# Performance work log

Hardware: AMD Instinct MI355X
Metric: run time of the kernel (lower is better)

## Reference

```python
import jax, jax.numpy as jnp
import numpy as np

N_INST = 100000
N_NET = 100000
E = 1600000
H = 64
OUT = 32
L = 2


def setup_inputs() -> dict:
    key = jax.random.key(0)
    ks = jax.random.split(key, 16)
    inp = {
        "x_inst": jax.random.normal(ks[0], (N_INST, H), jnp.float32),
        "x_net": jax.random.normal(ks[1], (N_NET, H), jnp.float32),
        "edge_i2n": jax.random.randint(ks[2], (2, E), 0, N_INST, jnp.int32),
        "edge_n2i": jax.random.randint(ks[3], (2, E), 0, N_NET, jnp.int32),
        # stacked GAT params: axis0 = layer, axis1 = relation (0: inst->net, 1: net->inst)
        "W_src": jax.random.normal(ks[4], (L, 2, H, H), jnp.float32) * 0.1,
        "W_dst": jax.random.normal(ks[5], (L, 2, H, H), jnp.float32) * 0.1,
        "att_src": jax.random.normal(ks[6], (L, 2, H), jnp.float32) * 0.1,
        "att_dst": jax.random.normal(ks[7], (L, 2, H), jnp.float32) * 0.1,
        "bias_g": jax.random.normal(ks[8], (L, 2, H), jnp.float32) * 0.1,
        "lin1_w": jax.random.normal(ks[9], (H, OUT), jnp.float32) * 0.1,
        "lin1_b": jax.random.normal(ks[10], (OUT,), jnp.float32) * 0.1,
        "lin2_w": jax.random.normal(ks[11], (OUT, 1), jnp.float32) * 0.1,
        "lin2_b": jax.random.normal(ks[12], (1,), jnp.float32) * 0.1,
    }
    return inp


def _segment_softmax(scores, seg, n_seg):
    # numerically stable softmax over edges grouped by destination node
    m = jax.ops.segment_max(scores, seg, num_segments=n_seg)
    e = jnp.exp(scores - m[seg])
    s = jax.ops.segment_sum(e, seg, num_segments=n_seg)
    return e / (s[seg] + 1e-16)


def _gat_conv(x_src, x_dst, edge, Ws, Wd, a_s, a_d, b, n_dst):
    # PyG GATConv, heads=1, add_self_loops=False, eval mode (dropout inactive)
    hs = x_src @ Ws  # [Ns, H]
    hd = x_dst @ Wd  # [Nd, H]
    src, dst = edge[0], edge[1]
    score = (hs * a_s).sum(-1)[src] + (hd * a_d).sum(-1)[dst]  # [E]
    alpha = _segment_softmax(jax.nn.leaky_relu(score, 0.2), dst, n_dst)
    out = jax.ops.segment_sum(hs[src] * alpha[:, None], dst, num_segments=n_dst)
    return out + b


def reference(x_inst, x_net, edge_i2n, edge_n2i, W_src, W_dst, att_src, att_dst,
              bias_g, lin1_w, lin1_b, lin2_w, lin2_b):
    xi, xn = x_inst, x_net
    for l in range(L):
        new_net = _gat_conv(xi, xn, edge_i2n, W_src[l, 0], W_dst[l, 0],
                            att_src[l, 0], att_dst[l, 0], bias_g[l, 0], xn.shape[0])
        new_inst = _gat_conv(xn, xi, edge_n2i, W_src[l, 1], W_dst[l, 1],
                             att_src[l, 1], att_dst[l, 1], bias_g[l, 1], xi.shape[0])
        xn = jax.nn.relu(new_net)
        xi = jax.nn.relu(new_inst)
    h = jax.nn.relu(xn @ lin1_w + lin1_b)
    return h @ lin2_w + lin2_b  # [N_net, 1]
```

## Files before the change

### kernel.cpp

```cpp
#include <hip/hip_runtime.h>
#include <hip/hip_fp16.h>

#define H 64
#define BSHIFT 9
#define BUCKET 512
#define NBMAX 256
#define CHUNK 4096

__device__ __forceinline__ int bcasti(int x, int j) {
    return __builtin_amdgcn_readlane(x, j);
}
__device__ __forceinline__ float bcastf(float x, int j) {
    return __uint_as_float((unsigned)__builtin_amdgcn_readlane((int)__float_as_uint(x), j));
}

__device__ __forceinline__ float ldf(const float* p) { return *p; }
__device__ __forceinline__ float ldf(const __half* p) { return __half2float(*p); }

__global__ void wvec3_kernel(const float* __restrict__ W_dst, const float* __restrict__ att_dst,
                             float* __restrict__ v2all) {
    int b = blockIdx.x;
    int k = threadIdx.x;
    const float* Wd = W_dst + (size_t)b * H * H;
    const float* ad = att_dst + (size_t)b * H;
    float s2 = 0.f;
    for (int j = 0; j < H; ++j) s2 += Wd[k * H + j] * ad[j];
    v2all[b * H + k] = s2;
}

template <typename T>
__device__ __forceinline__ void proj_body(float* __restrict__ Wl, int blk,
                                          const T* __restrict__ x, const float* __restrict__ W,
                                          const float* __restrict__ as_, const float* __restrict__ v2d,
                                          __half* __restrict__ hs, float* __restrict__ ssrc,
                                          float* __restrict__ sdst_out, int n) {
    int t = threadIdx.x;
    for (int i = t; i < H * H; i += 256) Wl[i] = W[i];
    __syncthreads();
    int lane = t & 63;
    int w = t >> 6;
    int row0 = blk * 16 + w * 4;
    if (row0 >= n) return;
    int rem = n - row0;
    float asl = as_[lane];
    const T* xp = x + (size_t)row0 * H + lane;
    float xr0 = ldf(xp);
    float xr1 = rem > 1 ? ldf(xp + H) : 0.f;
    float xr2 = rem > 2 ? ldf(xp + 2 * H) : 0.f;
    float xr3 = rem > 3 ? ldf(xp + 3 * H) : 0.f;
    float a0 = 0.f, a1 = 0.f, a2 = 0.f, a3 = 0.f;
#pragma unroll
    for (int k = 0; k < H; ++k) {
        float wv = Wl[k * H + lane];
        a0 = fmaf(bcastf(xr0, k), wv, a0);
        a1 = fmaf(bcastf(xr1, k), wv, a1);
        a2 = fmaf(bcastf(xr2, k), wv, a2);
        a3 = fmaf(bcastf(xr3, k), wv, a3);
    }
    __half* hp = hs + (size_t)row0 * H + lane;
    hp[0] = __float2half_rn(a0);
    if (rem > 1) hp[H] = __float2half_rn(a1);
    if (rem > 2) hp[2 * H] = __float2half_rn(a2);
    if (rem > 3) hp[3 * H] = __float2half_rn(a3);
    float p0 = a0 * asl, p1 = a1 * asl, p2 = a2 * asl, p3 = a3 * asl;
#pragma unroll
    for (int off = 32; off; off >>= 1) {
        p0 += __shfl_xor(p0, off); p1 += __shfl_xor(p1, off);
        p2 += __shfl_xor(p2, off); p3 += __shfl_xor(p3, off);
    }
    if (lane == 0) {
        ssrc[row0] = p0;
        if (rem > 1) ssrc[row0 + 1] = p1;
        if (rem > 2) ssrc[row0 + 2] = p2;
        if (rem > 3) ssrc[row0 + 3] = p3;
    }
    if (sdst_out) {
        float vl = v2d[lane];
        float q0 = xr0 * vl, q1 = xr1 * vl, q2 = xr2 * vl, q3 = xr3 * vl;
#pragma unroll
        for (int off = 32; off; off >>= 1) {
            q0 += __shfl_xor(q0, off); q1 += __shfl_xor(q1, off);
            q2 += __shfl_xor(q2, off); q3 += __shfl_xor(q3, off);
        }
        if (lane == 0) {
            sdst_out[row0] = q0;
            if (rem > 1) sdst_out[row0 + 1] = q1;
            if (rem > 2) sdst_out[row0 + 2] = q2;
            if (rem > 3) sdst_out[row0 + 3] = q3;
        }
    }
}

__global__ void hist_proj_kernel(const int* __restrict__ dstA, const int* __restrict__ dstB,
                                 int* __restrict__ cntA, int* __restrict__ cntB,
                                 int ne, int nch, int nbA, int nbB,
                                 const float* __restrict__ x, const float* __restrict__ W,
                                 const float* __restrict__ as_, const float* __restrict__ v2d,
                                 __half* __restrict__ hs, float* __restrict__ ssrc,
                                 float* __restrict__ sdst_out, int n) {
    __shared__ float smem[H * H];
    int blk = blockIdx.x;
    if (blk < 2 * nch) {
        int* h = (int*)smem;
        bool second = blk >= nch;
        const int* dst = second ? dstB : dstA;
        int* cnt = second ? cntB : cntA;
        int nb = second ? nbB : nbA;
        int c = second ? blk - nch : blk;
        int beg = c * CHUNK, end = beg + CHUNK;
        if (end > ne) end = ne;
        int t = threadIdx.x;
        for (int i = t; i < NBMAX; i += 256) h[i] = 0;
        __syncthreads();
        for (int i = beg + t; i < end; i += 256) atomicAdd(&h[dst[i] >> BSHIFT], 1);
        __syncthreads();
        for (int b = t; b < nb; b += 256) cnt[(size_t)b * nch + c] = h[b];
        return;
    }
    proj_body<float>(smem, blk - 2 * nch, x, W, as_, v2d, hs, ssrc, sdst_out, n);
}

__global__ void scan_chunks(int* __restrict__ cntA, int* __restrict__ cntB,
                            int* __restrict__ totA, int* __restrict__ totB,
                            int nch, int nbA) {
    __shared__ int sm[512];
    int b = blockIdx.x;
    bool second = b >= nbA;
    int* cnt = second ? cntB : cntA;
    int* tot = second ? totB : totA;
    if (second) b -= nbA;
    int t = threadIdx.x;
    int v = t < nch ? cnt[(size_t)b * nch + t] : 0;
    sm[t] = v;
    __syncthreads();
    for (int off = 1; off < 512; off <<= 1) {
        int u = t >= off ? sm[t - off] : 0;
        __syncthreads();
        sm[t] += u;
        __syncthreads();
    }
    if (t < nch) cnt[(size_t)b * nch + t] = sm[t] - v;
    if (t == 511) tot[b] = sm[511];
}

__global__ void scan_buckets(const int* __restrict__ totA, const int* __restrict__ totB,
                             int* __restrict__ bstartA, int* __restrict__ bstartB,
                             int nbA, int nbB, int ne) {
    __shared__ int sm[256];
    const int* tot = blockIdx.x ? totB : totA;
    int* bstart = blockIdx.x ? bstartB : bstartA;
    int nb = blockIdx.x ? nbB : nbA;
    int t = threadIdx.x;
    int v = t < nb ? tot[t] : 0;
    sm[t] = v;
    __syncthreads();
    for (int off = 1; off < 256; off <<= 1) {
        int u = t >= off ? sm[t - off] : 0;
        __syncthreads();
        sm[t] += u;
        __syncthreads();
    }
    if (t < nb) bstart[t] = sm[t] - v;
    if (t == 0) bstart[nb] = ne;
}

__global__ void scatter_proj_kernel(const int* __restrict__ srcA, const int* __restrict__ dstA,
                                    const int* __restrict__ cntA, const int* __restrict__ bstartA,
                                    unsigned* __restrict__ tmpA,
                                    const int* __restrict__ srcB, const int* __restrict__ dstB,
                                    const int* __restrict__ cntB, const int* __restrict__ bstartB,
                                    unsigned* __restrict__ tmpB,
                                    int ne, int nch, int nbA, int nbB,
                                    const float* __restrict__ x, const float* __restrict__ W,
                                    const float* __restrict__ as_, const float* __restrict__ v2d,
                                    __half* __restrict__ hs, float* __restrict__ ssrc,
                                    float* __restrict__ sdst_out, int n) {
    __shared__ float smem[H * H];
    int blk = blockIdx.x;
    if (blk < 2 * nch) {
        int* cur = (int*)smem;
        bool second = blk >= nch;
        const int* src = second ? srcB : srcA;
        const int* dst = second ? dstB : dstA;
        const int* cnt = second ? cntB : cntA;
        const int* bstart = second ? bstartB : bstartA;
        unsigned* tmp = second ? tmpB : tmpA;
        int nb = second ? nbB : nbA;
        int c = second ? blk - nch : blk;
        int beg = c * CHUNK, end = beg + CHUNK;
        if (end > ne) end = ne;
        int t = threadIdx.x;
        for (int b = t; b < nb; b += 256) cur[b] = bstart[b] + cnt[(size_t)b * nch + c];
        __syncthreads();
        for (int i = beg + t; i < end; i += 256) {
            int d = dst[i];
            int pos = atomicAdd(&cur[d >> BSHIFT], 1);
            unsigned rec = ((unsigned)(d & (BUCKET - 1)) << 17) | (unsigned)src[i];
            tmp[pos] = rec;
        }
        return;
    }
    proj_body<float>(smem, blk - 2 * nch, x, W, as_, v2d, hs, ssrc, sdst_out, n);
}

__global__ void bucket_finalize(const unsigned* __restrict__ tmpA, const int* __restrict__ bstartA,
                                int* __restrict__ rowptrA, int* __restrict__ srcsA,
                                int ndstA, int nbA,
                                const unsigned* __restrict__ tmpB, const int* __restrict__ bstartB,
                                int* __restrict__ rowptrB, int* __restrict__ srcsB,
                                int ndstB) {
    __shared__ int cnt[BUCKET];
    __shared__ int sm[BUCKET];
    __shared__ int cur[BUCKET];
    int b = blockIdx.x;
    bool second = b >= nbA;
    const unsigned* tmp = second ? tmpB : tmpA;
    const int* bstart = second ? bstartB : bstartA;
    int* rowptr = second ? rowptrB : rowptrA;
    int* srcs   = second ? srcsB : srcsA;
    int ndst    = second ? ndstB : ndstA;
    if (second) b -= nbA;

    int t = threadIdx.x;
    int base = bstart[b], endi = bstart[b + 1];
    cnt[t] = 0;
    __syncthreads();
    for (int i = base + t; i < endi; i += 512)
        atomicAdd(&cnt[tmp[i] >> 17], 1);
    __syncthreads();
    int c0 = cnt[t];
    sm[t] = c0;
    __syncthreads();
    for (int off = 1; off < 512; off <<= 1) {
        int u = t >= off ? sm[t - off] : 0;
        __syncthreads();
        sm[t] += u;
        __syncthreads();
    }
    int d0 = b << BSHIFT;
    int e = base + sm[t] - c0;
    cur[t] = e;
    if (d0 + t < ndst) rowptr[d0 + t] = e;
    if (t == 0) {
        int hi = d0 + BUCKET;
        if (hi > ndst) hi = ndst;
        rowptr[hi] = endi;
    }
    __syncthreads();
    for (int i = base + t; i < endi; i += 512) {
        unsigned rec = tmp[i];
        int pos = atomicAdd(&cur[rec >> 17], 1);
        srcs[pos] = (int)(rec & 0x1FFFFu);
    }
}

template <int P>
__device__ __forceinline__ float gat_fast(const int* __restrict__ srcs, int beg, int cnt,
                                          const float* __restrict__ ssrc, float sdst,
                                          const __half* __restrict__ hs,
                                          const float* __restrict__ bias, int lane) {
    bool valid = lane < cnt;
    int s_l = valid ? srcs[beg + lane] : 0;
    float ss = valid ? ssrc[s_l] : 0.f;

    const __half* hsl = hs + lane;
    __half hv[P];
#pragma unroll
    for (int k = 0; k < P; ++k) {
        hv[k] = hsl[(size_t)bcasti(s_l, k) * H];
    }

    float sc = ss + sdst;
    sc = sc > 0.f ? sc : 0.2f * sc;
    float ev_l = valid ? __expf(sc) : 0.f;
    float ll = ev_l;
#pragma unroll
    for (int off = 32; off; off >>= 1) ll += __shfl_xor(ll, off);

    float acc0 = 0.f, acc1 = 0.f, acc2 = 0.f, acc3 = 0.f;
    float acc4 = 0.f, acc5 = 0.f, acc6 = 0.f, acc7 = 0.f;
#pragma unroll
    for (int k = 0; k < P; k += 8) {
        acc0 += bcastf(ev_l, k + 0) * __half2float(hv[k + 0]);
        acc1 += bcastf(ev_l, k + 1) * __half2float(hv[k + 1]);
        acc2 += bcastf(ev_l, k + 2) * __half2float(hv[k + 2]);
        acc3 += bcastf(ev_l, k + 3) * __half2float(hv[k + 3]);
        acc4 += bcastf(ev_l, k + 4) * __half2float(hv[k + 4]);
        acc5 += bcastf(ev_l, k + 5) * __half2float(hv[k + 5]);
        acc6 += bcastf(ev_l, k + 6) * __half2float(hv[k + 6]);
        acc7 += bcastf(ev_l, k + 7) * __half2float(hv[k + 7]);
    }
    if constexpr (P == 32) {
        int j = P;
        for (; j + 3 < cnt; j += 4) {
            acc0 += bcastf(ev_l, j + 0) * __half2float(hsl[(size_t)bcasti(s_l, j + 0) * H]);
            acc1 += bcastf(ev_l, j + 1) * __half2float(hsl[(size_t)bcasti(s_l, j + 1) * H]);
            acc2 += bcastf(ev_l, j + 2) * __half2float(hsl[(size_t)bcasti(s_l, j + 2) * H]);
            acc3 += bcastf(ev_l, j + 3) * __half2float(hsl[(size_t)bcasti(s_l, j + 3) * H]);
        }
        for (; j < cnt; ++j)
            acc0 += bcastf(ev_l, j) * __half2float(hsl[(size_t)bcasti(s_l, j) * H]);
    }
    float v = ((acc0 + acc1) + (acc2 + acc3)) + ((acc4 + acc5) + (acc6 + acc7));
    v = v / (ll + 1e-16f) + bias[lane];
    return v > 0.f ? v : 0.f;
}

__device__ __forceinline__ float gat_aggregate(const int* __restrict__ rowptr,
                                               const int* __restrict__ srcs,
                                               const float* __restrict__ ssrc,
                                               float sdst,
                                               const __half* __restrict__ hs,
                                               const float* __restrict__ bias,
                                               int wid, int lane) {
    int beg = rowptr[wid], end = rowptr[wid + 1];
    int cnt = end - beg;
    if (cnt <= 16) return gat_fast<16>(srcs, beg, cnt, ssrc, sdst, hs, bias, lane);
    if (cnt <= 64) return gat_fast<32>(srcs, beg, cnt, ssrc, sdst, hs, bias, lane);

    const __half* hsl = hs + lane;
    float acc0 = 0.f, acc1 = 0.f;
    float mm = -3.4e38f;
    for (int base = beg; base < end; base += 64) {
        int idx = base + lane;
        if (idx < end) {
            float sc = ssrc[srcs[idx]] + sdst;
            sc = sc > 0.f ? sc : 0.2f * sc;
            mm = fmaxf(mm, sc);
        }
    }
#pragma unroll
    for (int off = 32; off; off >>= 1) mm = fmaxf(mm, __shfl_xor(mm, off));
    float ll = 0.f;
    for (int base = beg; base < end; base += 64) {
        int idx = base + lane;
        int c2 = end - base; if (c2 > 64) c2 = 64;
        int s_l = idx < end ? srcs[idx] : 0;
        float ev_l = 0.f;
        if (idx < end) {
            float sc = ssrc[s_l] + sdst;
            sc = sc > 0.f ? sc : 0.2f * sc;
            ev_l = __expf(sc - mm);
        }
        ll += ev_l;
        int j = 0;
        for (; j + 1 < c2; j += 2) {
            acc0 += bcastf(ev_l, j) * __half2float(hsl[(size_t)bcasti(s_l, j) * H]);
            acc1 += bcastf(ev_l, j + 1) * __half2float(hsl[(size_t)bcasti(s_l, j + 1) * H]);
        }
        if (j < c2)
            acc0 += bcastf(ev_l, j) * __half2float(hsl[(size_t)bcasti(s_l, j) * H]);
    }
#pragma unroll
    for (int off = 32; off; off >>= 1) ll += __shfl_xor(ll, off);
    float v = (acc0 + acc1) / (ll + 1e-16f) + bias[lane];
    return v > 0.f ? v : 0.f;
}

__global__ void gat1_kernel(const int* __restrict__ rp1, const int* __restrict__ sr1,
                            const float* __restrict__ ssrc1, const float* __restrict__ sdst1,
                            const __half* __restrict__ hs1, const float* __restrict__ bias1,
                            __half* __restrict__ out1, int n1) {
    int wid = (int)((blockIdx.x * blockDim.x + threadIdx.x) >> 6);
    int lane = threadIdx.x & 63;
    if (wid >= n1) return;
    float v = gat_aggregate(rp1, sr1, ssrc1, sdst1[wid], hs1, bias1, wid, lane);
    out1[(size_t)wid * H + lane] = __float2half_rn(v);
}

__global__ void gat0_proj_kernel(const int* __restrict__ rp0, const int* __restrict__ sr0,
                                 const float* __restrict__ ssrc0, const float* __restrict__ sdst0,
                                 const __half* __restrict__ hs0, const float* __restrict__ bias0,
                                 const float* __restrict__ v2next, float* __restrict__ sdstNext, int n0,
                                 const __half* __restrict__ xiA, const float* __restrict__ Wsrc2,
                                 const float* __restrict__ as2,
                                 __half* __restrict__ hs2, float* __restrict__ ssrc2, int n1) {
    __shared__ float smem[H * H];
    int nblk0 = (n0 + 3) / 4;
    if ((int)blockIdx.x < nblk0) {
        int wid = (int)((blockIdx.x * blockDim.x + threadIdx.x) >> 6);
        int lane = threadIdx.x & 63;
        if (wid >= n0) return;
        float v = gat_aggregate(rp0, sr0, ssrc0, sdst0[wid], hs0, bias0, wid, lane);
        float q = v * v2next[lane];
#pragma unroll
        for (int off = 32; off; off >>= 1) q += __shfl_xor(q, off);
        if (lane == 0) sdstNext[wid] = q;
        return;
    }
    proj_body<__half>(smem, blockIdx.x - nblk0, xiA, Wsrc2, as2, nullptr, hs2, ssrc2, nullptr, n1);
}

__global__ void gat_node_mlp_kernel(const int* __restrict__ rowptr, const int* __restrict__ srcs,
                                    const float* __restrict__ ssrc, const float* __restrict__ sdstArr,
                                    const __half* __restrict__ hs, const float* __restrict__ bias,
                                    const float* __restrict__ w1, const float* __restrict__ b1,
                                    const float* __restrict__ w2, const float* __restrict__ b2,
                                    float* __restrict__ out, int ndst) {
    __shared__ float W1[H * 32];
    __shared__ float W2[32];
    __shared__ float B1[32];
    {
        int t = threadIdx.x;
        for (int i = t; i < H * 32; i += 256) W1[i] = w1[i];
        if (t < 32) { W2[t] = w2[t]; B1[t] = b1[t]; }
        __syncthreads();
    }
    int wid = (int)((blockIdx.x * blockDim.x + threadIdx.x) >> 6);
    int lane = threadIdx.x & 63;
    if (wid >= ndst) return;
    float v = gat_aggregate(rowptr, srcs, ssrc, sdstArr[wid], hs, bias, wid, lane);

    int c = lane & 31;
    int kbase = (lane >> 5) << 5;
    float s = 0.f;
#pragma unroll
    for (int k = 0; k < 32; ++k) s += __shfl(v, kbase + k) * W1[(kbase + k) * 32 + c];
    s += __shfl_xor(s, 32);
    s += B1[c];
    s = s > 0.f ? s : 0.f;
    float q = s * W2[c];
#pragma unroll
    for (int off = 16; off; off >>= 1) q += __shfl_xor(q, off);
    if (lane == 0) out[wid] = q + b2[0];
}

extern "C" void kernel_launch(void* const* d_in, const int* in_sizes, int n_in,
                              void* d_out, int out_size, void* d_ws, size_t ws_size,
                              hipStream_t stream) {
    const float* x_inst  = (const float*)d_in[0];
    const float* x_net   = (const float*)d_in[1];
    const int*   e_i2n   = (const int*)d_in[2];
    const int*   e_n2i   = (const int*)d_in[3];
    const float* W_src   = (const float*)d_in[4];
    const float* W_dst   = (const float*)d_in[5];
    const float* att_src = (const float*)d_in[6];
    const float* att_dst = (const float*)d_in[7];
    const float* bias_g  = (const float*)d_in[8];
    const float* lin1_w  = (const float*)d_in[9];
    const float* lin1_b  = (const float*)d_in[10];
    const float* lin2_w  = (const float*)d_in[11];
    const float* lin2_b  = (const float*)d_in[12];

    const int n_inst = in_sizes[0] / H;
    const int n_net  = in_sizes[1] / H;
    const int ne     = in_sizes[2] / 2;
    const int nmax   = n_inst > n_net ? n_inst : n_net;

    const int nbA = (n_net + BUCKET - 1) >> BSHIFT;
    const int nbB = (n_inst + BUCKET - 1) >> BSHIFT;
    const int nch = (ne + CHUNK - 1) / CHUNK;

    float* ws = (float*)d_ws;
    size_t off = 0;
    auto alloc = [&](size_t nelem) {
        off = (off + 3) & ~(size_t)3;
        float* p = ws + off; off += nelem; return p;
    };
    __half* xiA    = (__half*)alloc((size_t)n_inst * H / 2);
    __half* hs0    = (__half*)alloc((size_t)nmax * H / 2);
    __half* hs1    = (__half*)alloc((size_t)nmax * H / 2);
    __half* hs2    = (__half*)alloc((size_t)nmax * H / 2);
    float* ssrc0   = alloc(nmax);
    float* ssrc1   = alloc(nmax);
    float* ssrc2   = alloc(nmax);
    float* sdstA   = alloc(nmax);
    float* sdstB   = alloc(nmax);
    float* sdstC   = alloc(nmax);
    int*   rp_i2n  = (int*)alloc(nmax + 1);
    int*   sr_i2n  = (int*)alloc(ne);
    int*   rp_n2i  = (int*)alloc(nmax + 1);
    int*   sr_n2i  = (int*)alloc(ne);
    unsigned* tmpA = (unsigned*)alloc(ne);
    unsigned* tmpB = (unsigned*)alloc(ne);
    int*   cntA    = (int*)alloc((size_t)NBMAX * nch);
    int*   cntB    = (int*)alloc((size_t)NBMAX * nch);
    int*   totA    = (int*)alloc(NBMAX);
    int*   totB    = (int*)alloc(NBMAX);
    int*   bstartA = (int*)alloc(NBMAX + 1);
    int*   bstartB = (int*)alloc(NBMAX + 1);
    float* v2all   = alloc(3 * H);
    (void)ws_size;

    const int* dstA = e_i2n + ne;
    const int* dstB = e_n2i + ne;

    wvec3_kernel<<<3, 64, 0, stream>>>(W_dst, att_dst, v2all);

    {
        int grid = 2 * nch + (n_inst + 15) / 16;
        hist_proj_kernel<<<grid, 256, 0, stream>>>(dstA, dstB, cntA, cntB, ne, nch, nbA, nbB,
                                                   x_inst, W_src + 0 * H * H, att_src + 0 * H,
                                                   v2all + 1 * H, hs0, ssrc0, sdstB, n_inst);
    }
    scan_chunks<<<nbA + nbB, 512, 0, stream>>>(cntA, cntB, totA, totB, nch, nbA);
    scan_buckets<<<2, 256, 0, stream>>>(totA, totB, bstartA, bstartB, nbA, nbB, ne);
    {
        int grid = 2 * nch + (n_net + 15) / 16;
        scatter_proj_kernel<<<grid, 256, 0, stream>>>(e_i2n, dstA, cntA, bstartA, tmpA,
                                                      e_n2i, dstB, cntB, bstartB, tmpB,
                                                      ne, nch, nbA, nbB,
                                                      x_net, W_src + 1 * H * H, att_src + 1 * H,
                                                      v2all + 0 * H, hs1, ssrc1, sdstA, n_net);
    }
    bucket_finalize<<<nbA + nbB, 512, 0, stream>>>(tmpA, bstartA, rp_i2n, sr_i2n, n_net, nbA,
                                                   tmpB, bstartB, rp_n2i, sr_n2i, n_inst);

    gat1_kernel<<<(n_inst + 3) / 4, 256, 0, stream>>>(rp_n2i, sr_n2i, ssrc1, sdstB,
                                                      hs1, bias_g + 1 * H, xiA, n_inst);
    {
        int grid = (n_net + 3) / 4 + (n_inst + 15) / 16;
        gat0_proj_kernel<<<grid, 256, 0, stream>>>(rp_i2n, sr_i2n, ssrc0, sdstA, hs0,
                                                   bias_g + 0 * H, v2all + 2 * H, sdstC, n_net,
                                                   xiA, W_src + 2 * H * H, att_src + 2 * H,
                                                   hs2, ssrc2, n_inst);
    }
    gat_node_mlp_kernel<<<(n_net + 3) / 4, 256, 0, stream>>>(rp_i2n, sr_i2n, ssrc2, sdstC,
                                                             hs2, bias_g + 2 * H,
                                                             lin1_w, lin1_b, lin2_w, lin2_b,
                                                             (float*)d_out, n_net);
}
```

Measured before the change: 330.9 us.

## Process two destination nodes per wavefront with half2 gathers in GAT aggregation

Layer-1 and layer-0 GAT aggregation kernels now assign two destination nodes to each 64-lane wavefront. Each 32-lane half handles one node and loads source rows as half2, so each lane computes two feature columns. Nodes with more than 32 in-edges fall back to the original per-node path, run serially within the wave. The goal is fewer idle lanes on low-degree nodes (average degree is about 16), wider memory accesses and fewer waves, at the cost of imbalance when the two paired nodes differ in degree.

```diff
diff --git a/kernel.cpp b/kernel.cpp
--- a/kernel.cpp
+++ b/kernel.cpp
@@ -306,6 +306,49 @@
     return v > 0.f ? v : 0.f;
 }
 
+__device__ __forceinline__ float gat_general(const int* __restrict__ srcs, int beg, int end,
+                                             const float* __restrict__ ssrc, float sdst,
+                                             const __half* __restrict__ hs,
+                                             const float* __restrict__ bias, int lane) {
+    const __half* hsl = hs + lane;
+    float acc0 = 0.f, acc1 = 0.f;
+    float mm = -3.4e38f;
+    for (int base = beg; base < end; base += 64) {
+        int idx = base + lane;
+        if (idx < end) {
+            float sc = ssrc[srcs[idx]] + sdst;
+            sc = sc > 0.f ? sc : 0.2f * sc;
+            mm = fmaxf(mm, sc);
+        }
+    }
+#pragma unroll
+    for (int off = 32; off; off >>= 1) mm = fmaxf(mm, __shfl_xor(mm, off));
+    float ll = 0.f;
+    for (int base = beg; base < end; base += 64) {
+        int idx = base + lane;
+        int c2 = end - base; if (c2 > 64) c2 = 64;
+        int s_l = idx < end ? srcs[idx] : 0;
+        float ev_l = 0.f;
+        if (idx < end) {
+            float sc = ssrc[s_l] + sdst;
+            sc = sc > 0.f ? sc : 0.2f * sc;
+            ev_l = __expf(sc - mm);
+        }
+        ll += ev_l;
+        int j = 0;
+        for (; j + 1 < c2; j += 2) {
+            acc0 += bcastf(ev_l, j) * __half2float(hsl[(size_t)bcasti(s_l, j) * H]);
+            acc1 += bcastf(ev_l, j + 1) * __half2float(hsl[(size_t)bcasti(s_l, j + 1) * H]);
+        }
+        if (j < c2)
+            acc0 += bcastf(ev_l, j) * __half2float(hsl[(size_t)bcasti(s_l, j) * H]);
+    }
+#pragma unroll
+    for (int off = 32; off; off >>= 1) ll += __shfl_xor(ll, off);
+    float v = (acc0 + acc1) / (ll + 1e-16f) + bias[lane];
+    return v > 0.f ? v : 0.f;
+}
+
 __device__ __forceinline__ float gat_aggregate(const int* __restrict__ rowptr,
                                                const int* __restrict__ srcs,
                                                const float* __restrict__ ssrc,
@@ -317,55 +360,99 @@
     int cnt = end - beg;
     if (cnt <= 16) return gat_fast<16>(srcs, beg, cnt, ssrc, sdst, hs, bias, lane);
     if (cnt <= 64) return gat_fast<32>(srcs, beg, cnt, ssrc, sdst, hs, bias, lane);
-
-    const __half* hsl = hs + lane;
-    float acc0 = 0.f, acc1 = 0.f;
-    float mm = -3.4e38f;
-    for (int base = beg; base < end; base += 64) {
-        int idx = base + lane;
-        if (idx < end) {
-            float sc = ssrc[srcs[idx]] + sdst;
-            sc = sc > 0.f ? sc : 0.2f * sc;
-            mm = fmaxf(mm, sc);
-        }
-    }
-#pragma unroll
-    for (int off = 32; off; off >>= 1) mm = fmaxf(mm, __shfl_xor(mm, off));
-    float ll = 0.f;
-    for (int base = beg; base < end; base += 64) {
-        int idx = base + lane;
-        int c2 = end - base; if (c2 > 64) c2 = 64;
-        int s_l = idx < end ? srcs[idx] : 0;
-        float ev_l = 0.f;
-        if (idx < end) {
-            float sc = ssrc[s_l] + sdst;
-            sc = sc > 0.f ? sc : 0.2f * sc;
-            ev_l = __expf(sc - mm);
-        }
-        ll += ev_l;
-        int j = 0;
-        for (; j + 1 < c2; j += 2) {
-            acc0 += bcastf(ev_l, j) * __half2float(hsl[(size_t)bcasti(s_l, j) * H]);
-            acc1 += bcastf(ev_l, j + 1) * __half2float(hsl[(size_t)bcasti(s_l, j + 1) * H]);
-        }
-        if (j < c2)
-            acc0 += bcastf(ev_l, j) * __half2float(hsl[(size_t)bcasti(s_l, j) * H]);
-    }
-#pragma unroll
-    for (int off = 32; off; off >>= 1) ll += __shfl_xor(ll, off);
-    float v = (acc0 + acc1) / (ll + 1e-16f) + bias[lane];
-    return v > 0.f ? v : 0.f;
-}
-
-__global__ void gat1_kernel(const int* __restrict__ rp1, const int* __restrict__ sr1,
-                            const float* __restrict__ ssrc1, const float* __restrict__ sdst1,
-                            const __half* __restrict__ hs1, const float* __restrict__ bias1,
-                            __half* __restrict__ out1, int n1) {
-    int wid = (int)((blockIdx.x * blockDim.x + threadIdx.x) >> 6);
-    int lane = threadIdx.x & 63;
-    if (wid >= n1) return;
-    float v = gat_aggregate(rp1, sr1, ssrc1, sdst1[wid], hs1, bias1, wid, lane);
-    out1[(size_t)wid * H + lane] = __float2half_rn(v);
+    return gat_general(srcs, beg, end, ssrc, sdst, hs, bias, lane);
+}
+
+template <int P>
+__device__ __forceinline__ float2 gat_pair_fast(const int* __restrict__ srcs,
+                                                int r0, int r1, int cnt0, int cnt1,
+                                                const float* __restrict__ ssrc,
+                                                float sdstA, float sdstB,
+                                                const __half* __restrict__ hs,
+                                                const float* __restrict__ bias,
+                                                int lane) {
+    int half = lane >> 5, sub = lane & 31;
+    int beg = half ? r1 : r0;
+    int cnt = half ? cnt1 : cnt0;
+    bool valid = sub < cnt;
+    int s_l = valid ? srcs[beg + sub] : 0;
+    float ss = valid ? ssrc[s_l] : 0.f;
+    float sdst = half ? sdstB : sdstA;
+
+    const __half2* hp = (const __half2*)hs;
+    __half2 hv[P];
+#pragma unroll
+    for (int k = 0; k < P; ++k) {
+        int sA = bcasti(s_l, k), sB = bcasti(s_l, 32 + k);
+        int srow = half ? sB : sA;
+        hv[k] = hp[(size_t)srow * 32 + sub];
+    }
+
+    float sc = ss + sdst;
+    sc = sc > 0.f ? sc : 0.2f * sc;
+    float ev_l = valid ? __expf(sc) : 0.f;
+    float ll = ev_l;
+#pragma unroll
+    for (int off = 16; off; off >>= 1) ll += __shfl_xor(ll, off);
+
+    float ax0 = 0.f, ax1 = 0.f, ax2 = 0.f, ax3 = 0.f;
+    float ay0 = 0.f, ay1 = 0.f, ay2 = 0.f, ay3 = 0.f;
+#pragma unroll
+    for (int k = 0; k < P; k += 4) {
+#pragma unroll
+        for (int u = 0; u < 4; ++u) {
+            float eA = bcastf(ev_l, k + u), eB = bcastf(ev_l, 32 + k + u);
+            float e = half ? eB : eA;
+            float2 f = __half22float2(hv[k + u]);
+            if (u == 0) { ax0 += e * f.x; ay0 += e * f.y; }
+            if (u == 1) { ax1 += e * f.x; ay1 += e * f.y; }
+            if (u == 2) { ax2 += e * f.x; ay2 += e * f.y; }
+            if (u == 3) { ax3 += e * f.x; ay3 += e * f.y; }
+        }
+    }
+    float vx = (ax0 + ax1) + (ax2 + ax3);
+    float vy = (ay0 + ay1) + (ay2 + ay3);
+    float inv = 1.f / (ll + 1e-16f);
+    float2 bv = *(const float2*)(bias + 2 * sub);
+    vx = vx * inv + bv.x;
+    vy = vy * inv + bv.y;
+    vx = vx > 0.f ? vx : 0.f;
+    vy = vy > 0.f ? vy : 0.f;
+    return make_float2(vx, vy);
+}
+
+__global__ void gat1_kernel(const int* __restrict__ rp, const int* __restrict__ sr,
+                            const float* __restrict__ ssrc, const float* __restrict__ sdstArr,
+                            const __half* __restrict__ hs, const float* __restrict__ bias,
+                            __half* __restrict__ out, int n) {
+    int t = (int)(blockIdx.x * blockDim.x + threadIdx.x);
+    int pw = t >> 6, lane = t & 63;
+    int wid0 = 2 * pw;
+    if (wid0 >= n) return;
+    bool has1 = wid0 + 1 < n;
+    int r0 = rp[wid0], r1 = rp[wid0 + 1];
+    int r2 = has1 ? rp[wid0 + 2] : r1;
+    int cnt0 = r1 - r0, cnt1 = r2 - r1;
+    int mx = cnt0 > cnt1 ? cnt0 : cnt1;
+    int half = lane >> 5, sub = lane & 31;
+
+    if (mx <= 32) {
+        float sdstA = sdstArr[wid0];
+        float sdstB = has1 ? sdstArr[wid0 + 1] : 0.f;
+        float2 v;
+        if (mx <= 16) v = gat_pair_fast<16>(sr, r0, r1, cnt0, cnt1, ssrc, sdstA, sdstB, hs, bias, lane);
+        else          v = gat_pair_fast<32>(sr, r0, r1, cnt0, cnt1, ssrc, sdstA, sdstB, hs, bias, lane);
+        int node = half ? wid0 + 1 : wid0;
+        if (!half || has1)
+            *(__half2*)(out + (size_t)node * H + 2 * sub) = __float22half2_rn(v);
+    } else {
+        float v0 = gat_aggregate(rp, sr, ssrc, sdstArr[wid0], hs, bias, wid0, lane);
+        out[(size_t)wid0 * H + lane] = __float2half_rn(v0);
+        if (has1) {
+            float v1 = gat_aggregate(rp, sr, ssrc, sdstArr[wid0 + 1], hs, bias, wid0 + 1, lane);
+            out[(size_t)(wid0 + 1) * H + lane] = __float2half_rn(v1);
+        }
+    }
 }
 
 __global__ void gat0_proj_kernel(const int* __restrict__ rp0, const int* __restrict__ sr0,
@@ -376,16 +463,46 @@
                                  const float* __restrict__ as2,
                                  __half* __restrict__ hs2, float* __restrict__ ssrc2, int n1) {
     __shared__ float smem[H * H];
-    int nblk0 = (n0 + 3) / 4;
+    int npair = (n0 + 1) / 2;
+    int nblk0 = (npair + 3) / 4;
     if ((int)blockIdx.x < nblk0) {
-        int wid = (int)((blockIdx.x * blockDim.x + threadIdx.x) >> 6);
-        int lane = threadIdx.x & 63;
-        if (wid >= n0) return;
-        float v = gat_aggregate(rp0, sr0, ssrc0, sdst0[wid], hs0, bias0, wid, lane);
-        float q = v * v2next[lane];
-#pragma unroll
-        for (int off = 32; off; off >>= 1) q += __shfl_xor(q, off);
-        if (lane == 0) sdstNext[wid] = q;
+        int t = (int)(blockIdx.x * blockDim.x + threadIdx.x);
+        int pw = t >> 6, lane = t & 63;
+        int wid0 = 2 * pw;
+        if (wid0 >= n0) return;
+        bool has1 = wid0 + 1 < n0;
+        int r0 = rp0[wid0], r1 = rp0[wid0 + 1];
+        int r2 = has1 ? rp0[wid0 + 2] : r1;
+        int cnt0 = r1 - r0, cnt1 = r2 - r1;
+        int mx = cnt0 > cnt1 ? cnt0 : cnt1;
+        int half = lane >> 5, sub = lane & 31;
+
+        if (mx <= 32) {
+            float sdA = sdst0[wid0];
+            float sdB = has1 ? sdst0[wid0 + 1] : 0.f;
+            float2 v;
+            if (mx <= 16) v = gat_pair_fast<16>(sr0, r0, r1, cnt0, cnt1, ssrc0, sdA, sdB, hs0, bias0, lane);
+            else          v = gat_pair_fast<32>(sr0, r0, r1, cnt0, cnt1, ssrc0, sdA, sdB, hs0, bias0, lane);
+            float2 w2 = *(const float2*)(v2next + 2 * sub);
+            float q = v.x * w2.x + v.y * w2.y;
+#pragma unroll
+            for (int off = 16; off; off >>= 1) q += __shfl_xor(q, off);
+            int node = half ? wid0 + 1 : wid0;
+            if (sub == 0 && (!half || has1)) sdstNext[node] = q;
+        } else {
+            float v0 = gat_aggregate(rp0, sr0, ssrc0, sdst0[wid0], hs0, bias0, wid0, lane);
+            float q0 = v0 * v2next[lane];
+#pragma unroll
+            for (int off = 32; off; off >>= 1) q0 += __shfl_xor(q0, off);
+            if (lane == 0) sdstNext[wid0] = q0;
+            if (has1) {
+                float v1 = gat_aggregate(rp0, sr0, ssrc0, sdst0[wid0 + 1], hs0, bias0, wid0 + 1, lane);
+                float q1 = v1 * v2next[lane];
+#pragma unroll
+                for (int off = 32; off; off >>= 1) q1 += __shfl_xor(q1, off);
+                if (lane == 0) sdstNext[wid0 + 1] = q1;
+            }
+        }
         return;
     }
     proj_body<__half>(smem, blockIdx.x - nblk0, xiA, Wsrc2, as2, nullptr, hs2, ssrc2, nullptr, n1);
@@ -506,10 +623,14 @@
     bucket_finalize<<<nbA + nbB, 512, 0, stream>>>(tmpA, bstartA, rp_i2n, sr_i2n, n_net, nbA,
                                                    tmpB, bstartB, rp_n2i, sr_n2i, n_inst);
 
-    gat1_kernel<<<(n_inst + 3) / 4, 256, 0, stream>>>(rp_n2i, sr_n2i, ssrc1, sdstB,
-                                                      hs1, bias_g + 1 * H, xiA, n_inst);
     {
-        int grid = (n_net + 3) / 4 + (n_inst + 15) / 16;
+        int npair = (n_inst + 1) / 2;
+        gat1_kernel<<<(npair + 3) / 4, 256, 0, stream>>>(rp_n2i, sr_n2i, ssrc1, sdstB,
+                                                         hs1, bias_g + 1 * H, xiA, n_inst);
+    }
+    {
+        int npair0 = (n_net + 1) / 2;
+        int grid = (npair0 + 3) / 4 + (n_inst + 15) / 16;
         gat0_proj_kernel<<<grid, 256, 0, stream>>>(rp_i2n, sr_i2n, ssrc0, sdstA, hs0,
                                                    bias_g + 0 * H, v2all + 2 * H, sdstC, n_net,
                                                    xiA, W_src + 2 * H * H, att_src + 2 * H,
```

Measured after the change: 327.9 us. Within noise of the previous version (-0.9%).
